# Kernel tuning notes

Hardware: AMD Instinct MI355X
Metric: run time of the kernel (lower is better)

## Reference

```python
import jax, jax.numpy as jnp
import numpy as np

GROUPS = 32
EPS = 1e-5
HEAD_DIM = 64


def group_norm(x, gamma, beta):
    # x: [B, L, C]; normalize over (L, C//G) within each of G channel groups
    B, L, C = x.shape
    g = x.reshape(B, L, GROUPS, C // GROUPS)
    mean = g.mean(axis=(1, 3), keepdims=True)
    var = g.var(axis=(1, 3), keepdims=True)
    g = (g - mean) * jax.lax.rsqrt(var + EPS)
    return g.reshape(B, L, C) * gamma + beta


def setup_inputs() -> dict:
    key = jax.random.key(0)
    ks = jax.random.split(key, 4)
    B, H, W, C = 16, 32, 32, 512
    x = jax.random.normal(ks[0], (B, H, W, C), dtype=jnp.float32)
    timesteps = jax.random.randint(ks[1], (B,), 0, 1000)
    gamma = jnp.ones((C,), jnp.float32)
    beta = jnp.zeros((C,), jnp.float32)
    w_qkv = jax.random.normal(ks[2], (C, 3 * C), dtype=jnp.float32) * (1.0 / np.sqrt(C))
    b_qkv = jnp.zeros((3 * C,), jnp.float32)
    w_out = jax.random.normal(ks[3], (C, C), dtype=jnp.float32) * (1.0 / np.sqrt(C))
    b_out = jnp.zeros((C,), jnp.float32)
    return {"x": x, "timesteps": timesteps, "gamma": gamma, "beta": beta,
            "w_qkv": w_qkv, "b_qkv": b_qkv, "w_out": w_out, "b_out": b_out}


def reference(x, timesteps, gamma, beta, w_qkv, b_qkv, w_out, b_out):
    B, H, W, C = x.shape
    L = H * W
    nh = C // HEAD_DIM
    factor = jnp.asarray(1.0 / np.sqrt(np.sqrt(HEAD_DIM)), x.dtype)  # applied to both q and k

    xf = x.reshape(B, L, C)
    qkv = group_norm(xf, gamma, beta) @ w_qkv + b_qkv        # [B, L, 3C]
    q, k, v = jnp.split(qkv, 3, axis=-1)

    def heads(t):  # [B, L, C] -> [B, nh, L, d]
        return t.reshape(B, L, nh, HEAD_DIM).transpose(0, 2, 1, 3)

    q, k, v = heads(q) * factor, heads(k) * factor, heads(v)
    scores = jnp.einsum('bhqd,bhkd->bhqk', q, k)             # [B, nh, L, L]
    attn = jax.nn.softmax(scores, axis=-1)
    out = jnp.einsum('bhqk,bhkd->bhqd', attn, v)             # [B, nh, L, d]
    out = out.transpose(0, 2, 1, 3).reshape(B, L, C)
    h = out @ w_out + b_out
    return (xf + h).reshape(B, H, W, C)
```

## Files before the change

### kernel.cpp

```cpp
#include <hip/hip_runtime.h>

#define Bn 16
#define Ln 1024
#define Cn 512
#define Mn (Bn*Ln)
#define N3n 1536

typedef unsigned short u16;
typedef __attribute__((ext_vector_type(8))) short short8;
typedef __attribute__((ext_vector_type(4))) float f32x4;
typedef __attribute__((ext_vector_type(16))) float f32x16;

typedef const __attribute__((address_space(1))) void* gas_p;
typedef __attribute__((address_space(3))) void* las_p;

__device__ inline void gl_lds16(const void* g, void* l) {
  __builtin_amdgcn_global_load_lds((gas_p)g, (las_p)l, 16, 0, 0);
}

__device__ inline u16 f2bf(float f) {
  union { float f; unsigned u; } v; v.f = f;
  unsigned r = v.u + 0x7FFFu + ((v.u >> 16) & 1u);
  return (u16)(r >> 16);
}

__device__ inline unsigned pk2(float a, float b) {
  return (__float_as_uint(a) >> 16) | (__float_as_uint(b) & 0xFFFF0000u);
}

__device__ inline f32x4 mfma16(short8 a, short8 b, f32x4 c) {
  return __builtin_amdgcn_mfma_f32_16x16x32_bf16(a, b, c, 0, 0, 0);
}
__device__ inline f32x16 mfma32(short8 a, short8 b, f32x16 c) {
  return __builtin_amdgcn_mfma_f32_32x32x16_bf16(a, b, c, 0, 0, 0);
}

__global__ __launch_bounds__(256) void k_gn(const float* __restrict__ x,
                                            const float* __restrict__ gamma,
                                            const float* __restrict__ beta,
                                            u16* __restrict__ gn) {
  __shared__ __attribute__((aligned(16))) float xs[1024 * 16];
  __shared__ float red[8];
  __shared__ float stat[2];
  int bid = blockIdx.x;
  int b = bid >> 5, g = bid & 31;
  const float* base = x + (size_t)b * (Ln * Cn) + g * 16;
  int tid = threadIdx.x;
  int c = tid & 3;
  float s1 = 0.f, s2 = 0.f;
  for (int i = 0; i < 16; ++i) {
    int s = i * 256 + tid;
    int r = s >> 2;
    float4 v = *(const float4*)(base + (size_t)r * Cn + c * 4);
    *(float4*)(xs + (size_t)s * 4) = v;
    s1 += v.x + v.y + v.z + v.w;
    s2 += v.x * v.x + v.y * v.y + v.z * v.z + v.w * v.w;
  }
  s1 += __shfl_xor(s1, 1);  s2 += __shfl_xor(s2, 1);
  s1 += __shfl_xor(s1, 2);  s2 += __shfl_xor(s2, 2);
  s1 += __shfl_xor(s1, 4);  s2 += __shfl_xor(s2, 4);
  s1 += __shfl_xor(s1, 8);  s2 += __shfl_xor(s2, 8);
  s1 += __shfl_xor(s1, 16); s2 += __shfl_xor(s2, 16);
  s1 += __shfl_xor(s1, 32); s2 += __shfl_xor(s2, 32);
  int w = tid >> 6, lane = tid & 63;
  if (lane == 0) { red[w] = s1; red[4 + w] = s2; }
  __syncthreads();
  if (tid == 0) {
    float a = red[0] + red[1] + red[2] + red[3];
    float q = red[4] + red[5] + red[6] + red[7];
    float mean = a * (1.f / 16384.f);
    float var = q * (1.f / 16384.f) - mean * mean;
    stat[0] = mean;
    stat[1] = rsqrtf(var + 1e-5f);
  }
  __syncthreads();
  float mean = stat[0], rstd = stat[1];
  float4 gv = *(const float4*)(gamma + g * 16 + c * 4);
  float4 bv = *(const float4*)(beta + g * 16 + c * 4);
  u16* gdst = gn + (size_t)b * (Ln * Cn) + g * 16;
  for (int i = 0; i < 16; ++i) {
    int s = i * 256 + tid;
    int r = s >> 2;
    float4 v = *(const float4*)(xs + (size_t)s * 4);
    ushort4 o;
    o.x = f2bf((v.x - mean) * rstd * gv.x + bv.x);
    o.y = f2bf((v.y - mean) * rstd * gv.y + bv.y);
    o.z = f2bf((v.z - mean) * rstd * gv.z + bv.z);
    o.w = f2bf((v.w - mean) * rstd * gv.w + bv.w);
    *(ushort4*)(gdst + (size_t)r * Cn + c * 4) = o;
  }
}

__global__ __launch_bounds__(256) void k_wtrans(const float* __restrict__ wqkv,
                                                const float* __restrict__ wout,
                                                u16* __restrict__ wqkvT,
                                                u16* __restrict__ woutT) {
  __shared__ float T[64][65];
  int bid = blockIdx.x;
  const float* src; u16* dst; int srcN, k0, n0;
  if (bid < 192) {
    src = wqkv; dst = wqkvT; srcN = 1536;
    int nt = bid % 24, kt = bid / 24;
    n0 = nt * 64; k0 = kt * 64;
  } else {
    int b2 = bid - 192;
    src = wout; dst = woutT; srcN = 512;
    int nt = b2 & 7, kt = b2 >> 3;
    n0 = nt * 64; k0 = kt * 64;
  }
  int tid = threadIdx.x;
  int r = tid >> 4, c4 = tid & 15;
#pragma unroll
  for (int i = 0; i < 4; ++i) {
    int rr = i * 16 + r;
    float4 v = *(const float4*)(src + (size_t)(k0 + rr) * srcN + n0 + c4 * 4);
    T[rr][c4 * 4 + 0] = v.x; T[rr][c4 * 4 + 1] = v.y;
    T[rr][c4 * 4 + 2] = v.z; T[rr][c4 * 4 + 3] = v.w;
  }
  __syncthreads();
  int r2 = tid >> 3, c2 = tid & 7;
#pragma unroll
  for (int i = 0; i < 2; ++i) {
    int nn = i * 32 + r2;
    int kk = c2 * 8;
    uint4 pk;
    pk.x = (unsigned)f2bf(T[kk + 0][nn]) | ((unsigned)f2bf(T[kk + 1][nn]) << 16);
    pk.y = (unsigned)f2bf(T[kk + 2][nn]) | ((unsigned)f2bf(T[kk + 3][nn]) << 16);
    pk.z = (unsigned)f2bf(T[kk + 4][nn]) | ((unsigned)f2bf(T[kk + 5][nn]) << 16);
    pk.w = (unsigned)f2bf(T[kk + 6][nn]) | ((unsigned)f2bf(T[kk + 7][nn]) << 16);
    *(uint4*)(dst + (size_t)(n0 + nn) * 512 + k0 + kk) = pk;
  }
}

__global__ __launch_bounds__(256) void k_qkv(const u16* __restrict__ gn,
                                             const u16* __restrict__ wT,
                                             const float* __restrict__ bias,
                                             u16* __restrict__ qb,
                                             u16* __restrict__ kb,
                                             u16* __restrict__ vT) {
  __shared__ __attribute__((aligned(16))) char smem[66560];
  int bid = blockIdx.x;
  int wg = (bid & 7) * 192 + (bid >> 3);
  int tn = wg % 12, tm = wg / 12;
  int m0 = tm * 128, n0 = tn * 128;
  int tid = threadIdx.x;
  int w = tid >> 6, lane = tid & 63, lr = lane & 15, lg = lane >> 4;
  int wr = w >> 1, wc = w & 1;
  const f32x4 fzero = {0.f, 0.f, 0.f, 0.f};
  f32x4 acc[4][4];
#pragma unroll
  for (int mi = 0; mi < 4; ++mi)
#pragma unroll
    for (int ni = 0; ni < 4; ++ni) acc[mi][ni] = fzero;

#pragma unroll
  for (int i = 0; i < 4; ++i) {
    int s = i * 256 + tid;
    int r = s >> 3, c = s & 7;
    gl_lds16(gn + ((size_t)(m0 + r) * 512 + ((c ^ (r & 7)) << 3)),
             smem + ((s & ~63) << 4));
    gl_lds16(wT + ((size_t)(n0 + r) * 512 + ((c ^ (r & 7)) << 3)),
             smem + 32768 + ((s & ~63) << 4));
  }
  __syncthreads();

  for (int kt = 0; kt < 8; ++kt) {
    int cur = kt & 1;
    char* Asb = smem + cur * 16384;
    char* Bsb = smem + 32768 + cur * 16384;
    if (kt < 7) {
      int nb = cur ^ 1, k0n = (kt + 1) * 64;
#pragma unroll
      for (int i = 0; i < 4; ++i) {
        int s = i * 256 + tid;
        int r = s >> 3, c = s & 7;
        gl_lds16(gn + ((size_t)(m0 + r) * 512 + k0n + ((c ^ (r & 7)) << 3)),
                 smem + nb * 16384 + ((s & ~63) << 4));
        gl_lds16(wT + ((size_t)(n0 + r) * 512 + k0n + ((c ^ (r & 7)) << 3)),
                 smem + 32768 + nb * 16384 + ((s & ~63) << 4));
      }
    }
#pragma unroll
    for (int ks = 0; ks < 2; ++ks) {
      short8 af[4], bf[4];
#pragma unroll
      for (int mi = 0; mi < 4; ++mi) {
        int row = wr * 64 + mi * 16 + lr;
        int ck = ks * 4 + lg;
        af[mi] = *(const short8*)(Asb + row * 128 + ((ck ^ (lr & 7)) << 4));
      }
#pragma unroll
      for (int ni = 0; ni < 4; ++ni) {
        int row = wc * 64 + ni * 16 + lr;
        int ck = ks * 4 + lg;
        bf[ni] = *(const short8*)(Bsb + row * 128 + ((ck ^ (lr & 7)) << 4));
      }
#pragma unroll
      for (int mi = 0; mi < 4; ++mi)
#pragma unroll
        for (int ni = 0; ni < 4; ++ni)
          acc[mi][ni] = mfma16(af[mi], bf[ni], acc[mi][ni]);
    }
    __syncthreads();
  }

  if (tn >= 8) {
    float* T = (float*)smem;
#pragma unroll
    for (int mi = 0; mi < 4; ++mi)
#pragma unroll
      for (int ni = 0; ni < 4; ++ni) {
        int n_l = wc * 64 + ni * 16 + lr;
        float bn = bias[n0 + n_l];
#pragma unroll
        for (int rr = 0; rr < 4; ++rr) {
          int m_l = wr * 64 + mi * 16 + lg * 4 + rr;
          T[n_l * 130 + m_l] = acc[mi][ni][rr] + bn;
        }
      }
    __syncthreads();
    int n_l = tid >> 1, half = tid & 1;
    int nv = n0 - 1024 + n_l;
    int h = nv >> 6, dd = nv & 63;
    int bb = m0 >> 10, li0 = m0 & 1023;
    u16* dst = vT + ((size_t)(bb * 8 + h) * 64 + dd) * 1024 + li0;
    const float* Tr = T + n_l * 130;
#pragma unroll
    for (int j = 0; j < 8; ++j) {
      int mb = half * 8 + 16 * j;
      uint4 o;
      o.x = (unsigned)f2bf(Tr[mb + 0]) | ((unsigned)f2bf(Tr[mb + 1]) << 16);
      o.y = (unsigned)f2bf(Tr[mb + 2]) | ((unsigned)f2bf(Tr[mb + 3]) << 16);
      o.z = (unsigned)f2bf(Tr[mb + 4]) | ((unsigned)f2bf(Tr[mb + 5]) << 16);
      o.w = (unsigned)f2bf(Tr[mb + 6]) | ((unsigned)f2bf(Tr[mb + 7]) << 16);
      *(uint4*)(dst + mb) = o;
    }
  } else {
#pragma unroll
    for (int mi = 0; mi < 4; ++mi) {
#pragma unroll
      for (int ni = 0; ni < 4; ++ni) {
        int n = n0 + wc * 64 + ni * 16 + lr;
        float bn = bias[n];
        int which = n >> 9, nn = n & 511;
        int h = nn >> 6, dd = nn & 63;
#pragma unroll
        for (int rr = 0; rr < 4; ++rr) {
          int m = m0 + wr * 64 + mi * 16 + lg * 4 + rr;
          float v = acc[mi][ni][rr] + bn;
          int bb = m >> 10, li = m & 1023;
          if (which == 0)
            qb[((size_t)(bb * 8 + h) * 1024 + li) * 64 + dd] = f2bf(v);
          else
            kb[((size_t)(bb * 8 + h) * 1024 + li) * 64 + dd] = f2bf(v);
        }
      }
    }
  }
}

__global__ __launch_bounds__(512, 4) void k_attn(const u16* __restrict__ qb,
                                                 const u16* __restrict__ kb,
                                                 const u16* __restrict__ vT,
                                                 u16* __restrict__ ob) {
  __shared__ __attribute__((aligned(16))) u16 Ks[3 * 64 * 64];
  __shared__ __attribute__((aligned(16))) u16 Vs[3 * 64 * 64];
  int bid = blockIdx.x;
  int xq = bid & 7, kk = bid >> 3;
  int bh = ((kk & 15) << 3) | xq;
  int qt = kk >> 4;
  const u16* qh = qb + (size_t)bh * 65536;
  const u16* kh = kb + (size_t)bh * 65536;
  const u16* vh = vT + (size_t)bh * 65536;
  int tid = threadIdx.x, w = tid >> 6, lane = tid & 63;
  int l31 = lane & 31, lhi = lane >> 5;
  int q0 = qt * 256 + w * 32;
  const float C1 = 0.18033688011112042f;

  short8 qf[4];
#pragma unroll
  for (int ks = 0; ks < 4; ++ks)
    qf[ks] = *(const short8*)(qh + (size_t)(q0 + l31) * 64 + ks * 16 + lhi * 8);

  f32x16 accO[2];
#pragma unroll
  for (int dt = 0; dt < 2; ++dt)
#pragma unroll
    for (int r = 0; r < 16; ++r) accO[dt][r] = 0.f;
  float lst = 0.f;

  int sr = tid >> 3, sc8 = tid & 7;
  size_t koff = (size_t)sr * 64 + ((sc8 ^ (sr & 7)) << 3);
  size_t voff = (size_t)sr * 1024 + ((sc8 ^ (sr & 7)) << 3);
  int ldst = (tid & ~63) << 4;

  gl_lds16(kh + koff, (char*)Ks + ldst);
  gl_lds16(vh + voff, (char*)Vs + ldst);
  gl_lds16(kh + 4096 + koff, (char*)Ks + 8192 + ldst);
  gl_lds16(vh + 64 + voff, (char*)Vs + 8192 + ldst);
  asm volatile("s_waitcnt vmcnt(2)" ::: "memory");
  __builtin_amdgcn_s_barrier();

#pragma unroll 1
  for (int jt = 0; jt < 16; ++jt) {
    int cb = jt % 3;
    char* Ksb = (char*)Ks + cb * 8192;
    char* Vsb = (char*)Vs + cb * 8192;
    if (jt < 14) {
      int nb = (jt + 2) % 3;
      gl_lds16(kh + (size_t)(jt + 2) * 4096 + koff, (char*)Ks + nb * 8192 + ldst);
      gl_lds16(vh + (size_t)(jt + 2) * 64 + voff, (char*)Vs + nb * 8192 + ldst);
    }

    f32x16 sc0, sc1;
#pragma unroll
    for (int r = 0; r < 16; ++r) { sc0[r] = 0.f; sc1[r] = 0.f; }
    __builtin_amdgcn_s_setprio(1);
#pragma unroll
    for (int ks = 0; ks < 4; ++ks) {
      int row = l31;
      short8 kf = *(const short8*)(Ksb + row * 128 + (((2 * ks + lhi) ^ (row & 7)) << 4));
      sc0 = mfma32(kf, qf[ks], sc0);
    }
#pragma unroll
    for (int ks = 0; ks < 4; ++ks) {
      int row = 32 + l31;
      short8 kf = *(const short8*)(Ksb + row * 128 + (((2 * ks + lhi) ^ (row & 7)) << 4));
      sc1 = mfma32(kf, qf[ks], sc1);
    }
    __builtin_amdgcn_s_setprio(0);

    float rs = 0.f;
#pragma unroll
    for (int r = 0; r < 16; ++r) {
      float pp = __builtin_amdgcn_exp2f(sc0[r] * C1);
      sc0[r] = pp; rs += pp;
    }
#pragma unroll
    for (int r = 0; r < 16; ++r) {
      float pp = __builtin_amdgcn_exp2f(sc1[r] * C1);
      sc1[r] = pp; rs += pp;
    }
    lst += rs;

    short8 ap[4];
#pragma unroll
    for (int kt2 = 0; kt2 < 2; ++kt2) {
#pragma unroll
      for (int hh = 0; hh < 2; ++hh) {
        unsigned A0, A1, B0, B1;
        if (kt2 == 0) {
          A0 = pk2(sc0[8 * hh + 0], sc0[8 * hh + 1]);
          A1 = pk2(sc0[8 * hh + 2], sc0[8 * hh + 3]);
          B0 = pk2(sc0[8 * hh + 4], sc0[8 * hh + 5]);
          B1 = pk2(sc0[8 * hh + 6], sc0[8 * hh + 7]);
        } else {
          A0 = pk2(sc1[8 * hh + 0], sc1[8 * hh + 1]);
          A1 = pk2(sc1[8 * hh + 2], sc1[8 * hh + 3]);
          B0 = pk2(sc1[8 * hh + 4], sc1[8 * hh + 5]);
          B1 = pk2(sc1[8 * hh + 6], sc1[8 * hh + 7]);
        }
        unsigned t0 = lhi ? A0 : B0;
        unsigned t1 = lhi ? A1 : B1;
        unsigned xt0 = __shfl_xor(t0, 32);
        unsigned xt1 = __shfl_xor(t1, 32);
        union { uint4 u; short8 s; } cv;
        cv.u.x = lhi ? xt0 : A0;
        cv.u.y = lhi ? xt1 : A1;
        cv.u.z = lhi ? B0 : xt0;
        cv.u.w = lhi ? B1 : xt1;
        ap[2 * kt2 + hh] = cv.s;
      }
    }

    __builtin_amdgcn_s_setprio(1);
#pragma unroll
    for (int ks2 = 0; ks2 < 4; ++ks2) {
#pragma unroll
      for (int dt = 0; dt < 2; ++dt) {
        int row = dt * 32 + l31;
        short8 bv = *(const short8*)(Vsb + row * 128 + (((2 * ks2 + lhi) ^ (row & 7)) << 4));
        accO[dt] = mfma32(ap[ks2], bv, accO[dt]);
      }
    }
    __builtin_amdgcn_s_setprio(0);

    if (jt < 14)
      asm volatile("s_waitcnt vmcnt(2)" ::: "memory");
    else
      asm volatile("s_waitcnt vmcnt(0)" ::: "memory");
    __builtin_amdgcn_s_barrier();
  }

  int b = bh >> 3, h = bh & 7;
  float lt = lst + __shfl_xor(lst, 32);
  float il = 1.f / lt;
#pragma unroll
  for (int reg = 0; reg < 16; ++reg) {
    int qrow = (reg & 3) + 8 * (reg >> 2) + 4 * lhi;
    float ib = __shfl(il, qrow);
    int row = q0 + qrow;
#pragma unroll
    for (int dt = 0; dt < 2; ++dt) {
      int col = h * 64 + dt * 32 + l31;
      ob[(size_t)(b * 1024 + row) * 512 + col] = f2bf(accO[dt][reg] * ib);
    }
  }
}

__global__ __launch_bounds__(256) void k_out(const u16* __restrict__ ob,
                                             const u16* __restrict__ wT,
                                             const float* __restrict__ bias,
                                             const float* __restrict__ x,
                                             float* __restrict__ out) {
  __shared__ __attribute__((aligned(16))) u16 As[2 * 128 * 64];
  __shared__ __attribute__((aligned(16))) u16 Bs[2 * 128 * 64];
  int bid = blockIdx.x;
  int wg = (bid & 7) * 64 + (bid >> 3);
  int tn = wg & 3, tm = wg >> 2;
  int m0 = tm * 128, n0 = tn * 128;
  int tid = threadIdx.x;
  int w = tid >> 6, lane = tid & 63, lr = lane & 15, lg = lane >> 4;
  int wr = w >> 1, wc = w & 1;
  const f32x4 fzero = {0.f, 0.f, 0.f, 0.f};
  f32x4 acc[4][4];
#pragma unroll
  for (int mi = 0; mi < 4; ++mi)
#pragma unroll
    for (int ni = 0; ni < 4; ++ni) acc[mi][ni] = fzero;

#pragma unroll
  for (int i = 0; i < 4; ++i) {
    int s = i * 256 + tid;
    int r = s >> 3, c = s & 7;
    gl_lds16(ob + ((size_t)(m0 + r) * 512 + ((c ^ (r & 7)) << 3)),
             (char*)As + ((s & ~63) << 4));
    gl_lds16(wT + ((size_t)(n0 + r) * 512 + ((c ^ (r & 7)) << 3)),
             (char*)Bs + ((s & ~63) << 4));
  }
  __syncthreads();

  for (int kt = 0; kt < 8; ++kt) {
    int cur = kt & 1;
    char* Asb = (char*)As + cur * 16384;
    char* Bsb = (char*)Bs + cur * 16384;
    if (kt < 7) {
      int nb = cur ^ 1, k0n = (kt + 1) * 64;
#pragma unroll
      for (int i = 0; i < 4; ++i) {
        int s = i * 256 + tid;
        int r = s >> 3, c = s & 7;
        gl_lds16(ob + ((size_t)(m0 + r) * 512 + k0n + ((c ^ (r & 7)) << 3)),
                 (char*)As + nb * 16384 + ((s & ~63) << 4));
        gl_lds16(wT + ((size_t)(n0 + r) * 512 + k0n + ((c ^ (r & 7)) << 3)),
                 (char*)Bs + nb * 16384 + ((s & ~63) << 4));
      }
    }
#pragma unroll
    for (int ks = 0; ks < 2; ++ks) {
      short8 af[4], bf[4];
#pragma unroll
      for (int mi = 0; mi < 4; ++mi) {
        int row = wr * 64 + mi * 16 + lr;
        int ck = ks * 4 + lg;
        af[mi] = *(const short8*)(Asb + row * 128 + ((ck ^ (lr & 7)) << 4));
      }
#pragma unroll
      for (int ni = 0; ni < 4; ++ni) {
        int row = wc * 64 + ni * 16 + lr;
        int ck = ks * 4 + lg;
        bf[ni] = *(const short8*)(Bsb + row * 128 + ((ck ^ (lr & 7)) << 4));
      }
#pragma unroll
      for (int mi = 0; mi < 4; ++mi)
#pragma unroll
        for (int ni = 0; ni < 4; ++ni)
          acc[mi][ni] = mfma16(af[mi], bf[ni], acc[mi][ni]);
    }
    __syncthreads();
  }
#pragma unroll
  for (int mi = 0; mi < 4; ++mi) {
#pragma unroll
    for (int ni = 0; ni < 4; ++ni) {
      int n = n0 + wc * 64 + ni * 16 + lr;
      float bn = bias[n];
#pragma unroll
      for (int rr = 0; rr < 4; ++rr) {
        int m = m0 + wr * 64 + mi * 16 + lg * 4 + rr;
        size_t off = (size_t)m * 512 + n;
        out[off] = x[off] + acc[mi][ni][rr] + bn;
      }
    }
  }
}

extern "C" void kernel_launch(void* const* d_in, const int* in_sizes, int n_in,
                              void* d_out, int out_size, void* d_ws, size_t ws_size,
                              hipStream_t stream) {
  const float* x = (const float*)d_in[0];
  const float* gamma = (const float*)d_in[2];
  const float* beta = (const float*)d_in[3];
  const float* wqkv = (const float*)d_in[4];
  const float* bqkv = (const float*)d_in[5];
  const float* wout = (const float*)d_in[6];
  const float* bout = (const float*)d_in[7];
  float* out = (float*)d_out;

  char* ws = (char*)d_ws;
  u16* gn = (u16*)(ws + 4096);
  u16* wqkvT = (u16*)(ws + 4096 + 16777216);
  u16* woutT = (u16*)(ws + 4096 + 16777216 + 1572864);
  u16* qb = (u16*)(ws + 4096 + 16777216 + 1572864 + 524288);
  u16* kb = qb + 8388608;
  u16* vT = kb + 8388608;
  u16* ob = vT + 8388608;

  k_gn<<<512, 256, 0, stream>>>(x, gamma, beta, gn);
  k_wtrans<<<256, 256, 0, stream>>>(wqkv, wout, wqkvT, woutT);
  k_qkv<<<1536, 256, 0, stream>>>(gn, wqkvT, bqkv, qb, kb, vT);
  k_attn<<<512, 512, 0, stream>>>(qb, kb, vT, ob);
  k_out<<<512, 256, 0, stream>>>(ob, woutT, bout, x, out);
}
```

Baseline: 122.5 us.

## Permute V storage order to drop cross-lane shuffles in P·V operand build

The V-transpose epilogue now writes key positions in a permuted order, where bits 2 and 3 of the index are swapped within each 16-block. The attention kernel can then pack the exponentiated score registers straight into MFMA A-operands with no __shfl_xor exchanges between half-waves. The s_setprio hints around the MFMA blocks are also removed. Correctness depends on the permutation matching the MFMA 32x32 output register layout exactly for both P and V.

```diff
diff --git a/kernel.cpp b/kernel.cpp
--- a/kernel.cpp
+++ b/kernel.cpp
@@ -228,11 +228,13 @@
 #pragma unroll
     for (int j = 0; j < 8; ++j) {
       int mb = half * 8 + 16 * j;
+#define SIG(IDX) (((IDX) & ~15) | (((IDX) & 4) << 1) | (((IDX) & 8) >> 1) | ((IDX) & 3))
       uint4 o;
-      o.x = (unsigned)f2bf(Tr[mb + 0]) | ((unsigned)f2bf(Tr[mb + 1]) << 16);
-      o.y = (unsigned)f2bf(Tr[mb + 2]) | ((unsigned)f2bf(Tr[mb + 3]) << 16);
-      o.z = (unsigned)f2bf(Tr[mb + 4]) | ((unsigned)f2bf(Tr[mb + 5]) << 16);
-      o.w = (unsigned)f2bf(Tr[mb + 6]) | ((unsigned)f2bf(Tr[mb + 7]) << 16);
+      o.x = (unsigned)f2bf(Tr[SIG(mb + 0)]) | ((unsigned)f2bf(Tr[SIG(mb + 1)]) << 16);
+      o.y = (unsigned)f2bf(Tr[SIG(mb + 2)]) | ((unsigned)f2bf(Tr[SIG(mb + 3)]) << 16);
+      o.z = (unsigned)f2bf(Tr[SIG(mb + 4)]) | ((unsigned)f2bf(Tr[SIG(mb + 5)]) << 16);
+      o.w = (unsigned)f2bf(Tr[SIG(mb + 6)]) | ((unsigned)f2bf(Tr[SIG(mb + 7)]) << 16);
+#undef SIG
       *(uint4*)(dst + mb) = o;
     }
   } else {
@@ -315,7 +317,6 @@
     f32x16 sc0, sc1;
 #pragma unroll
     for (int r = 0; r < 16; ++r) { sc0[r] = 0.f; sc1[r] = 0.f; }
-    __builtin_amdgcn_s_setprio(1);
 #pragma unroll
     for (int ks = 0; ks < 4; ++ks) {
       int row = l31;
@@ -328,7 +329,6 @@
       short8 kf = *(const short8*)(Ksb + row * 128 + (((2 * ks + lhi) ^ (row & 7)) << 4));
       sc1 = mfma32(kf, qf[ks], sc1);
     }
-    __builtin_amdgcn_s_setprio(0);
 
     float rs = 0.f;
 #pragma unroll
@@ -344,36 +344,22 @@
     lst += rs;
 
     short8 ap[4];
-#pragma unroll
-    for (int kt2 = 0; kt2 < 2; ++kt2) {
-#pragma unroll
-      for (int hh = 0; hh < 2; ++hh) {
-        unsigned A0, A1, B0, B1;
-        if (kt2 == 0) {
-          A0 = pk2(sc0[8 * hh + 0], sc0[8 * hh + 1]);
-          A1 = pk2(sc0[8 * hh + 2], sc0[8 * hh + 3]);
-          B0 = pk2(sc0[8 * hh + 4], sc0[8 * hh + 5]);
-          B1 = pk2(sc0[8 * hh + 6], sc0[8 * hh + 7]);
-        } else {
-          A0 = pk2(sc1[8 * hh + 0], sc1[8 * hh + 1]);
-          A1 = pk2(sc1[8 * hh + 2], sc1[8 * hh + 3]);
-          B0 = pk2(sc1[8 * hh + 4], sc1[8 * hh + 5]);
-          B1 = pk2(sc1[8 * hh + 6], sc1[8 * hh + 7]);
-        }
-        unsigned t0 = lhi ? A0 : B0;
-        unsigned t1 = lhi ? A1 : B1;
-        unsigned xt0 = __shfl_xor(t0, 32);
-        unsigned xt1 = __shfl_xor(t1, 32);
-        union { uint4 u; short8 s; } cv;
-        cv.u.x = lhi ? xt0 : A0;
-        cv.u.y = lhi ? xt1 : A1;
-        cv.u.z = lhi ? B0 : xt0;
-        cv.u.w = lhi ? B1 : xt1;
-        ap[2 * kt2 + hh] = cv.s;
-      }
-    }
-
-    __builtin_amdgcn_s_setprio(1);
+    {
+      union { uint4 u; short8 s; } cv;
+      cv.u.x = pk2(sc0[0], sc0[1]);  cv.u.y = pk2(sc0[2], sc0[3]);
+      cv.u.z = pk2(sc0[4], sc0[5]);  cv.u.w = pk2(sc0[6], sc0[7]);
+      ap[0] = cv.s;
+      cv.u.x = pk2(sc0[8], sc0[9]);  cv.u.y = pk2(sc0[10], sc0[11]);
+      cv.u.z = pk2(sc0[12], sc0[13]); cv.u.w = pk2(sc0[14], sc0[15]);
+      ap[1] = cv.s;
+      cv.u.x = pk2(sc1[0], sc1[1]);  cv.u.y = pk2(sc1[2], sc1[3]);
+      cv.u.z = pk2(sc1[4], sc1[5]);  cv.u.w = pk2(sc1[6], sc1[7]);
+      ap[2] = cv.s;
+      cv.u.x = pk2(sc1[8], sc1[9]);  cv.u.y = pk2(sc1[10], sc1[11]);
+      cv.u.z = pk2(sc1[12], sc1[13]); cv.u.w = pk2(sc1[14], sc1[15]);
+      ap[3] = cv.s;
+    }
+
 #pragma unroll
     for (int ks2 = 0; ks2 < 4; ++ks2) {
 #pragma unroll
@@ -383,7 +369,6 @@
         accO[dt] = mfma32(ap[ks2], bv, accO[dt]);
       }
     }
-    __builtin_amdgcn_s_setprio(0);
 
     if (jt < 14)
       asm volatile("s_waitcnt vmcnt(2)" ::: "memory");
```

New measurement: 118.2 us. -3.5%, faster.
